# Performance work log

Hardware: AMD Instinct MI355X
Metric: run time of the kernel (lower is better)

## Reference

```python
import jax, jax.numpy as jnp
import numpy as np

B, T, F, H, FUT = 64, 512, 64, 512, 96  # batch, past len, features, hidden, future len


def setup_inputs() -> dict:
    key = jax.random.key(0)
    ks = jax.random.split(key, 19)
    s = 1.0 / np.sqrt(H)  # PyTorch LSTM/Linear init scale
    u = lambda k, shape: jax.random.uniform(k, shape, jnp.float32, -s, s)
    inp = {"input_seq": jax.random.normal(ks[0], (B, T, F), jnp.float32)}
    i = 1
    for pre in ("enc", "dec"):
        for l in range(2):
            ins = F if l == 0 else H
            inp[f"{pre}_Wih{l}"] = u(ks[i], (4 * H, ins)); i += 1
            inp[f"{pre}_Whh{l}"] = u(ks[i], (4 * H, H)); i += 1
            inp[f"{pre}_bih{l}"] = u(ks[i], (4 * H,)); i += 1
            inp[f"{pre}_bhh{l}"] = u(ks[i], (4 * H,)); i += 1
    inp["fc_W"] = u(ks[17], (F, H))
    inp["fc_b"] = u(ks[18], (F,))
    return inp


def _cell(x, h, c, Wih, Whh, bih, bhh):
    # PyTorch gate order: i, f, g, o
    g = x @ Wih.T + h @ Whh.T + bih + bhh
    i_, f_, g_, o_ = jnp.split(g, 4, axis=-1)
    c = jax.nn.sigmoid(f_) * c + jax.nn.sigmoid(i_) * jnp.tanh(g_)
    h = jax.nn.sigmoid(o_) * jnp.tanh(c)
    return h, c


def reference(input_seq, enc_Wih0, enc_Whh0, enc_bih0, enc_bhh0,
              enc_Wih1, enc_Whh1, enc_bih1, enc_bhh1,
              dec_Wih0, dec_Whh0, dec_bih0, dec_bhh0,
              dec_Wih1, dec_Whh1, dec_bih1, dec_bhh1,
              fc_W, fc_b):
    b = input_seq.shape[0]
    z = jnp.zeros((b, H), input_seq.dtype)

    def run_layer(x, Wih, Whh, bih, bhh):
        def step(carry, xt):
            h, c = _cell(xt, carry[0], carry[1], Wih, Whh, bih, bhh)
            return (h, c), h
        (h, c), ys = jax.lax.scan(step, (z, z), jnp.swapaxes(x, 0, 1))
        return jnp.swapaxes(ys, 0, 1), h, c

    # encoder (2 layers, eval mode -> no dropout)
    y0, h0, c0 = run_layer(input_seq, enc_Wih0, enc_Whh0, enc_bih0, enc_bhh0)
    _, h1, c1 = run_layer(y0, enc_Wih1, enc_Whh1, enc_bih1, enc_bhh1)

    def dec_step(carry, _):
        x, dh0, dc0, dh1, dc1 = carry
        dh0, dc0 = _cell(x, dh0, dc0, dec_Wih0, dec_Whh0, dec_bih0, dec_bhh0)
        dh1, dc1 = _cell(dh0, dh1, dc1, dec_Wih1, dec_Whh1, dec_bih1, dec_bhh1)
        out = dh1 @ fc_W.T + fc_b
        return (out, dh0, dc0, dh1, dc1), out

    dec_in = input_seq[:, -1, :]
    _, outs = jax.lax.scan(dec_step, (dec_in, h0, c0, h1, c1), None, length=FUT)
    return jnp.swapaxes(outs, 0, 1)  # [B, FUT, F]
```

## Files before the change

kernel.cpp:

```cpp
#include <hip/hip_runtime.h>
#include <stdint.h>

typedef __attribute__((ext_vector_type(8))) short short8;
typedef __attribute__((ext_vector_type(4))) float floatx4;
typedef unsigned short u16;
typedef unsigned int u32;

constexpr int BSZ = 64;
constexpr int SEQT = 512;
constexpr int FIN = 64;
constexpr int HID = 512;
constexpr int NG = 2048;
constexpr int FUTL = 96;
constexpr int K0 = FIN + HID;
constexpr int K1 = HID + HID;
constexpr int K0P = K0 + 8;
constexpr int NGRP = 256;
constexpr int NFCB = 4;
constexpr int NBLK = NGRP + NFCB;
constexpr int NTHR = 256;

constexpr int SLOT_HP = 128 * 256;
constexpr int SLOT_XP = 16 * 256;
constexpr int NSLOT_H = 65;

constexpr size_t S_W0 = (size_t)NG * K0 * 2;
constexpr size_t S_W1 = (size_t)NG * K1 * 2;
constexpr size_t S_FC = (size_t)FIN * HID * 2;

constexpr size_t OFF_WHI_E0 = 0;
constexpr size_t OFF_WLO_E0 = OFF_WHI_E0 + S_W0;
constexpr size_t OFF_WHI_E1 = OFF_WLO_E0 + S_W0;
constexpr size_t OFF_WLO_E1 = OFF_WHI_E1 + S_W1;
constexpr size_t OFF_WHI_D1 = OFF_WLO_E1 + S_W1;
constexpr size_t OFF_WLO_D1 = OFF_WHI_D1 + S_W1;
constexpr size_t OFF_WFH   = OFF_WLO_D1 + S_W1;
constexpr size_t OFF_WFL   = OFF_WFH + S_W1;
constexpr size_t OFF_FCHI  = OFF_WFL + S_W1;
constexpr size_t OFF_FCLO  = OFF_FCHI + S_FC;
constexpr size_t OFF_GX    = OFF_FCLO + S_FC;
constexpr size_t OFF_BEFF  = OFF_GX + (size_t)NG * BSZ * 4;
constexpr size_t OFF_XP    = OFF_BEFF + (size_t)NG * 4;
constexpr size_t OFF_H0P   = OFF_XP + (size_t)SEQT * SLOT_XP * 4;
constexpr size_t OFF_H1P   = OFF_H0P + (size_t)NSLOT_H * SLOT_HP * 4;
constexpr size_t OFF_CNT   = OFF_H1P + (size_t)NSLOT_H * SLOT_HP * 4;
constexpr size_t CNT_BYTES = 65536;

#define FCF(c)   ((c) + 0)
#define DONE0(c) ((c) + 256)
#define DONE1(c) ((c) + 2304)
#define GOA0(c)  ((c) + 4352)
#define GOB0(c)  ((c) + 6400)
#define GOA1(c)  ((c) + 8448)
#define GOB1(c)  ((c) + 10496)

__device__ __forceinline__ u16 f2bf(float f) {
  u32 u = __float_as_uint(f);
  u += 0x7FFFu + ((u >> 16) & 1u);
  return (u16)(u >> 16);
}
__device__ __forceinline__ float bf2f(u16 h) { return __uint_as_float(((u32)h) << 16); }
__device__ __forceinline__ u32 packsplit(float v) {
  u16 h = f2bf(v);
  u16 l = f2bf(v - bf2f(h));
  return (u32)h | ((u32)l << 16);
}

__device__ __forceinline__ float sigf(float x) { return 1.f / (1.f + __expf(-x)); }
__device__ __forceinline__ float tanh_f(float x) {
  float xx = fminf(20.f, fmaxf(-20.f, x));
  float e = __expf(-2.f * xx);
  return (1.f - e) / (1.f + e);
}

__device__ __forceinline__ floatx4 mfma3(short8 ah, short8 al, short8 bh, short8 bl, floatx4 acc) {
  acc = __builtin_amdgcn_mfma_f32_16x16x32_bf16(ah, bh, acc, 0, 0, 0);
  acc = __builtin_amdgcn_mfma_f32_16x16x32_bf16(ah, bl, acc, 0, 0, 0);
  acc = __builtin_amdgcn_mfma_f32_16x16x32_bf16(al, bh, acc, 0, 0, 0);
  return acc;
}

__device__ __forceinline__ void st_sc_u32(u32* p, u32 v) {
  asm volatile("global_store_dword %0, %1, off sc0 sc1" :: "v"(p), "v"(v) : "memory");
}
#define WAITVM0() asm volatile("s_waitcnt vmcnt(0)" ::: "memory")

#define ALD(p) __hip_atomic_load((p), __ATOMIC_RELAXED, __HIP_MEMORY_SCOPE_AGENT)
#define AST(p, v) __hip_atomic_store((p), (v), __ATOMIC_RELAXED, __HIP_MEMORY_SCOPE_AGENT)

__device__ __forceinline__ int slotof(int u) { return u < 0 ? 0 : ((u & 63) + 1); }

__device__ __forceinline__ void ld_frag(const u32* p, short8& ah, short8& al) {
  uint4 a = *(const uint4*)p;
  uint4 b = *(const uint4*)(p + 256);
  union { u32 u[4]; short8 s; } H, L;
  H.u[0] = __builtin_amdgcn_perm(a.y, a.x, 0x05040100u);
  L.u[0] = __builtin_amdgcn_perm(a.y, a.x, 0x07060302u);
  H.u[1] = __builtin_amdgcn_perm(a.w, a.z, 0x05040100u);
  L.u[1] = __builtin_amdgcn_perm(a.w, a.z, 0x07060302u);
  H.u[2] = __builtin_amdgcn_perm(b.y, b.x, 0x05040100u);
  L.u[2] = __builtin_amdgcn_perm(b.y, b.x, 0x07060302u);
  H.u[3] = __builtin_amdgcn_perm(b.w, b.z, 0x05040100u);
  L.u[3] = __builtin_amdgcn_perm(b.w, b.z, 0x07060302u);
  ah = H.s; al = L.s;
}

__global__ void k_split_pair(const float* __restrict__ Wih, const float* __restrict__ Whh,
                             int ins, int K, u16* __restrict__ hi, u16* __restrict__ lo) {
  int n = NG * K;
  for (int idx = blockIdx.x * blockDim.x + threadIdx.x; idx < n; idx += gridDim.x * blockDim.x) {
    int row = idx / K;
    int k = idx - row * K;
    float v = (k < ins) ? Wih[row * ins + k] : Whh[row * HID + (k - ins)];
    u16 h = f2bf(v);
    hi[idx] = h;
    lo[idx] = f2bf(v - bf2f(h));
  }
}

__global__ void k_split_flat(const float* __restrict__ src, u16* __restrict__ hi,
                             u16* __restrict__ lo, int n) {
  for (int idx = blockIdx.x * blockDim.x + threadIdx.x; idx < n; idx += gridDim.x * blockDim.x) {
    float v = src[idx];
    u16 h = f2bf(v);
    hi[idx] = h;
    lo[idx] = f2bf(v - bf2f(h));
  }
}

__global__ void k_fuse(const float* __restrict__ dWih0, const float* __restrict__ dWhh0,
                       const float* __restrict__ fcW,
                       u16* __restrict__ wfh, u16* __restrict__ wfl) {
  __shared__ float wr[FIN];
  const int row = blockIdx.x;
  if (threadIdx.x < FIN) wr[threadIdx.x] = dWih0[row * FIN + threadIdx.x];
  __syncthreads();
  for (int j = threadIdx.x; j < HID; j += blockDim.x) {
    float acc = 0.f;
#pragma unroll
    for (int f = 0; f < FIN; ++f) acc = fmaf(wr[f], fcW[f * HID + j], acc);
    u16 h = f2bf(acc);
    wfh[(size_t)row * K1 + j] = h;
    wfl[(size_t)row * K1 + j] = f2bf(acc - bf2f(h));
    float v2 = dWhh0[row * HID + j];
    u16 h2 = f2bf(v2);
    wfh[(size_t)row * K1 + HID + j] = h2;
    wfl[(size_t)row * K1 + HID + j] = f2bf(v2 - bf2f(h2));
  }
}

__global__ void k_gx(const float* __restrict__ dWih0, const float* __restrict__ in_seq,
                     const float* __restrict__ fcb, const float* __restrict__ bdih0,
                     const float* __restrict__ bdhh0, float* __restrict__ gx,
                     float* __restrict__ beff) {
  __shared__ float xl[BSZ * FIN];
  __shared__ float fb[FIN];
  const int row0 = blockIdx.x * 8;
  for (int i = threadIdx.x; i < BSZ * FIN; i += blockDim.x) {
    int b = i >> 6, f = i & 63;
    xl[i] = in_seq[(b * SEQT + (SEQT - 1)) * FIN + f];
  }
  if (threadIdx.x < FIN) fb[threadIdx.x] = fcb[threadIdx.x];
  __syncthreads();
  for (int i = threadIdx.x; i < 8 * BSZ; i += blockDim.x) {
    int r = row0 + (i >> 6);
    int b = i & 63;
    float acc = 0.f;
#pragma unroll 8
    for (int f = 0; f < FIN; ++f)
      acc = fmaf(dWih0[r * FIN + f], xl[(b << 6) + f] - fb[f], acc);
    gx[r * BSZ + b] = acc;
    if (b == 0) {
      float accb = 0.f;
#pragma unroll 8
      for (int f = 0; f < FIN; ++f) accb = fmaf(dWih0[r * FIN + f], fb[f], accb);
      beff[r] = bdih0[r] + bdhh0[r] + accb;
    }
  }
}

__global__ void k_pack_x(const float* __restrict__ x, u32* __restrict__ xp) {
  int n = BSZ * SEQT * FIN;
  for (int idx = blockIdx.x * blockDim.x + threadIdx.x; idx < n; idx += gridDim.x * blockDim.x) {
    int t = idx / (BSZ * FIN);
    int rem = idx - t * (BSZ * FIN);
    int b = rem >> 6;
    int f = rem & 63;
    u32 pk = packsplit(x[(b * SEQT + t) * FIN + f]);
    int off = ((f >> 2) * 64 + b) * 4 + (f & 3);
    xp[t * SLOT_XP + off] = pk;
  }
}

struct Params {
  const u16 *we0h, *we0l, *we1h, *we1l;
  const u16 *wd1h, *wd1l, *wfh, *wfl;
  const u16 *fch, *fcl;
  const u32 *xp;
  u32 *h0p, *h1p;
  const float *beih0, *behh0, *beih1, *behh1;
  const float *bdih1, *bdhh1;
  const float *gx, *beff;
  const float *fcb;
  float *out;
  u32 *cnt;
};

__device__ void master_wait(u32* own, u32 ownT) {
  if (threadIdx.x < 64) {
    int l = threadIdx.x;
    while (!__all(ALD(own + l * 16) >= ownT && ALD(own + (l + 64) * 16) >= ownT)) {}
  }
  __syncthreads();
}

__device__ void sweep128(u32* arr, u32 T) {
  if (threadIdx.x < 64) {
    int l = threadIdx.x;
    while (!__all(ALD(arr + l * 16) >= T && ALD(arr + (l + 64) * 16) >= T))
      __builtin_amdgcn_s_sleep(1);
  }
  __syncthreads();
}

__device__ __forceinline__ void worker_wait(u32* cell, u32 tok) {
  if (threadIdx.x == 0) {
    while (ALD(cell) < tok) {}
  }
  __syncthreads();
}

__device__ __forceinline__ void worker_wait_c(u32* cell, u32 tok, u32& cache) {
  if (threadIdx.x == 0 && cache < tok) {
    u32 v;
    do { v = ALD(cell); } while (v < tok);
    cache = v;
  }
  __syncthreads();
}

__device__ __forceinline__ void fcf_wait_c(u32* fcf, u32 tok, u32& cache) {
  if (threadIdx.x == 0 && cache < tok) {
    u32 m;
    do {
      u32 a = ALD(fcf), b = ALD(fcf + 16), c = ALD(fcf + 32), d = ALD(fcf + 48);
      u32 m1 = a < b ? a : b, m2 = c < d ? c : d;
      m = m1 < m2 ? m1 : m2;
    } while (m < tok);
    cache = m;
  }
  __syncthreads();
}

__device__ __forceinline__ void fence_acq() {
  __builtin_amdgcn_fence(__ATOMIC_ACQUIRE, "agent");
}

__device__ __forceinline__ void arrive(u32* cell, u32 tok) {
  WAITVM0();
  __syncthreads();
  if (threadIdx.x == 0) AST(cell, tok);
}

__device__ __forceinline__ void bcast(u32* goA, u32 tokA, u32* goBF, u32 prog) {
  const int tid = threadIdx.x;
  if (tid >= 1 && tid < 128) AST(goA + (tid << 4), tokA);
  else if (tid >= 128) AST(goBF + ((tid - 128) << 4), prog);
}

template <bool IS_L1>
__device__ void load_w_lds(const u16* __restrict__ gh, const u16* __restrict__ gl,
                           u16* wh, u16* wl, int hc) {
  constexpr int K = IS_L1 ? K1 : K0;
  for (int i = threadIdx.x; i < 16 * K; i += NTHR) {
    int rr, k;
    if (IS_L1) { rr = i >> 10; k = i & 1023; }
    else       { rr = i / K0;  k = i - rr * K0; }
    int gc = ((rr >> 2) * HID) + hc + (rr & 3);
    int dst = IS_L1 ? ((rr << 10) + ((((k >> 3) ^ rr)) << 3) + (k & 7))
                    : (rr * K0P + k);
    wh[dst] = gh[(size_t)gc * K + k];
    wl[dst] = gl[(size_t)gc * K + k];
  }
  __syncthreads();
}

template <bool IS_L1, int KBASE, int LEN>
__device__ __forceinline__ void kpart(const u32* __restrict__ sp,
                                      const u16* __restrict__ wh, const u16* __restrict__ wl,
                                      int r, int quad, int mo, floatx4& acc) {
  const int qo = quad << 3;
  constexpr int NIT = LEN / 32;
  uint4 ra[NIT], rb[NIT];
#pragma unroll
  for (int i = 0; i < NIT; ++i) {
    const u32* p = sp + (((i * 32 + qo) >> 2) << 8) + mo;
    ra[i] = *(const uint4*)p;
    rb[i] = *(const uint4*)(p + 256);
  }
#pragma unroll
  for (int i = 0; i < NIT; ++i) {
    union { u32 u[4]; short8 s; } H, L;
    H.u[0] = __builtin_amdgcn_perm(ra[i].y, ra[i].x, 0x05040100u);
    L.u[0] = __builtin_amdgcn_perm(ra[i].y, ra[i].x, 0x07060302u);
    H.u[1] = __builtin_amdgcn_perm(ra[i].w, ra[i].z, 0x05040100u);
    L.u[1] = __builtin_amdgcn_perm(ra[i].w, ra[i].z, 0x07060302u);
    H.u[2] = __builtin_amdgcn_perm(rb[i].y, rb[i].x, 0x05040100u);
    L.u[2] = __builtin_amdgcn_perm(rb[i].y, rb[i].x, 0x07060302u);
    H.u[3] = __builtin_amdgcn_perm(rb[i].w, rb[i].z, 0x05040100u);
    L.u[3] = __builtin_amdgcn_perm(rb[i].w, rb[i].z, 0x07060302u);
    const int kg = i * 32 + KBASE;
    int woff;
    if (IS_L1) { int c = (kg >> 3) + quad; woff = (r << 10) + ((c ^ r) << 3); }
    else       { woff = r * K0P + kg + qo; }
    short8 bh = *(const short8*)(wh + woff);
    short8 bl = *(const short8*)(wl + woff);
    acc = mfma3(H.s, L.s, bh, bl, acc);
  }
}

__device__ __forceinline__ void epilogue(floatx4 acc, floatx4 bs, float& creg,
                                         u32* __restrict__ oslab,
                                         const float* __restrict__ gxb) {
  const int tid = threadIdx.x, lane = tid & 63;
  const int j = lane & 3;
  const int isel = (lane >> 2) & 3;
  const int slb = lane & 48;
  float gate[4];
#pragma unroll
  for (int q = 0; q < 4; ++q) {
    const int sl = slb + (q << 2) + j;
    float t0 = __shfl(acc[0], sl, 64);
    float t1 = __shfl(acc[1], sl, 64);
    float t2 = __shfl(acc[2], sl, 64);
    float t3 = __shfl(acc[3], sl, 64);
    gate[q] = (isel == 0) ? t0 : (isel == 1) ? t1 : (isel == 2) ? t2 : t3;
  }
  if (gxb != nullptr) {
    const int bb = tid >> 2;
#pragma unroll
    for (int q = 0; q < 4; ++q) gate[q] += gxb[q * (HID * BSZ) + j * BSZ + bb];
  }
  float iv = gate[0] + bs[0];
  float fv = gate[1] + bs[1];
  float gv = gate[2] + bs[2];
  float ov = gate[3] + bs[3];
  float cn = fmaf(sigf(fv), creg, sigf(iv) * tanh_f(gv));
  float hn = sigf(ov) * tanh_f(cn);
  creg = cn;
  st_sc_u32(oslab + tid, packsplit(hn));
}

__device__ void fc_step(int t, int blkq, const u32* __restrict__ h1slot,
                        const u16* __restrict__ fh, const u16* __restrict__ fl,
                        const float* __restrict__ fcb, float* __restrict__ out) {
  const int tid = threadIdx.x, lane = tid & 63, w = tid >> 6;
  const int quad = lane >> 4, r = lane & 15;
  const int m = (w << 4) + r;
  const int qo = quad << 3;
  const int mo = m << 2;
  const int col = (blkq << 4) + r;
  floatx4 acc = {0.f, 0.f, 0.f, 0.f};
#pragma unroll
  for (int kk = 0; kk < HID; kk += 32) {
    short8 ah, al;
    ld_frag(h1slot + (((kk + qo) >> 2) << 8) + mo, ah, al);
    short8 b1 = *(const short8*)(fh + col * HID + kk + qo);
    short8 b2 = *(const short8*)(fl + col * HID + kk + qo);
    acc = mfma3(ah, al, b1, b2, acc);
  }
  float bias = fcb[col];
#pragma unroll
  for (int i = 0; i < 4; ++i) {
    int b = (w << 4) + (quad << 2) + i;
    out[(b * FUTL + t) * FIN + col] = acc[i] + bias;
  }
}

__global__ __launch_bounds__(NTHR, 1) void lstm_coop(Params p) {
  __shared__ u16 wsmem[32768];
  u16* wh = wsmem;
  u16* wl = wsmem + 16 * 1024;
  const int blk = blockIdx.x;
  const int tid = threadIdx.x;

  u32* fcf = FCF(p.cnt);
  u32* d0 = DONE0(p.cnt);
  u32* d1 = DONE1(p.cnt);

  if (blk >= NGRP) {
    const int fi = blk - NGRP;
    for (int t = 0; t < FUTL; ++t) {
      sweep128(d1, (u32)(513 + t));
      if ((t & 63) == 0) fence_acq();
      fc_step(t, fi, p.h1p + (size_t)slotof(512 + t) * SLOT_HP,
              p.fch, p.fcl, p.fcb, p.out);
      WAITVM0();
      __syncthreads();
      if (tid == 0) AST(fcf + fi * 16, (u32)(t + 1));
    }
    return;
  }

  const int grp = blk >> 7;
  const int lidx = blk & 127;
  const int hc = lidx << 2;
  const int lane = tid & 63, w = tid >> 6;
  const int quad = lane >> 4, r = lane & 15;
  const int mo = ((w << 4) + r) << 2;

  u32* goA  = grp ? GOA1(p.cnt) : GOA0(p.cnt);
  u32* goBF = grp ? GOB0(p.cnt) : GOB1(p.cnt);
  u32* myGoA = goA + lidx * 16;
  u32* myGoB = (grp ? GOB1(p.cnt) : GOB0(p.cnt)) + lidx * 16;
  u32* myDone = (grp ? d1 : d0) + lidx * 16;

  floatx4 bse, bsd;
  {
    int ch = hc + (tid & 3);
    const float* bi  = grp ? p.beih1 : p.beih0;
    const float* bh2 = grp ? p.behh1 : p.behh0;
#pragma unroll
    for (int q = 0; q < 4; ++q) {
      bse[q] = bi[q * HID + ch] + bh2[q * HID + ch];
      bsd[q] = grp ? (p.bdih1[q * HID + ch] + p.bdhh1[q * HID + ch])
                   : p.beff[q * HID + ch];
    }
  }
  float creg = 0.f;

  if (!grp) {
    u32 d1seen = 0;
    load_w_lds<false>(p.we0h, p.we0l, wh, wl, hc);
    for (int s = 0; s < SEQT; ++s) {
      u32 tok = (u32)(s + 1);
      floatx4 acc = {0.f, 0.f, 0.f, 0.f};
      if (lidx == 0) {
        master_wait(d0, (u32)s);
        if (s >= 63) worker_wait_c(myGoB, (u32)(s - 63), d1seen);
        bcast(goA, tok, goBF, (u32)s);
        if ((s & 63) == 0 && s) fence_acq();
        kpart<false, 0, FIN>(p.xp + (size_t)s * SLOT_XP, wh, wl, r, quad, mo, acc);
      } else {
        kpart<false, 0, FIN>(p.xp + (size_t)s * SLOT_XP, wh, wl, r, quad, mo, acc);
        worker_wait(myGoA, tok);
        if ((s & 63) == 0 && s) fence_acq();
      }
      kpart<false, FIN, HID>(p.h0p + (size_t)slotof(s - 1) * SLOT_HP, wh, wl, r, quad, mo, acc);
      epilogue(acc, bse, creg,
               p.h0p + (size_t)slotof(s) * SLOT_HP + (lidx << 8), nullptr);
      arrive(myDone, tok);
    }
    if (lidx == 0) {
      sweep128(d0, 512u);
      if (tid >= 128) AST(goBF + ((tid - 128) << 4), 512u);
    }
    load_w_lds<true>(p.wfh, p.wfl, wh, wl, hc);
    for (int t = 0; t < FUTL; ++t) {
      u32 tok = (u32)(513 + t);
      floatx4 acc = {0.f, 0.f, 0.f, 0.f};
      if (lidx == 0) {
        master_wait(d0, (u32)(512 + t));
        if (t == 0) worker_wait_c(myGoB, 449u, d1seen);
        bcast(goA, tok, goBF, (u32)(512 + t));
      } else {
        worker_wait(myGoA, tok);
      }
      if ((t & 63) == 0) fence_acq();
      kpart<true, 512, HID>(p.h0p + (size_t)slotof(511 + t) * SLOT_HP, wh, wl, r, quad, mo, acc);
      if (t) {
        worker_wait_c(myGoB, (u32)(512 + t), d1seen);
        kpart<true, 0, HID>(p.h1p + (size_t)slotof(511 + t) * SLOT_HP, wh, wl, r, quad, mo, acc);
      }
      epilogue(acc, bsd, creg,
               p.h0p + (size_t)slotof(512 + t) * SLOT_HP + (lidx << 8),
               (t == 0) ? (p.gx + hc * BSZ) : nullptr);
      arrive(myDone, tok);
    }
    if (lidx == 0) {
      sweep128(d0, 608u);
      if (tid >= 128) AST(goBF + ((tid - 128) << 4), 608u);
    }
  } else {
    u32 d0seen = 0;
    u32 fcseen = 0;
    load_w_lds<true>(p.we1h, p.we1l, wh, wl, hc);
    for (int t = 0; t < SEQT; ++t) {
      u32 tok = (u32)(t + 1);
      floatx4 acc = {0.f, 0.f, 0.f, 0.f};
      if (lidx == 0) {
        master_wait(d1, (u32)t);
        bcast(goA, tok, goBF, (u32)t);
        worker_wait_c(myGoB, (u32)(t + 1), d0seen);
        if ((t & 63) == 0 && t) fence_acq();
        kpart<true, 0, HID>(p.h0p + (size_t)slotof(t) * SLOT_HP, wh, wl, r, quad, mo, acc);
        kpart<true, 512, HID>(p.h1p + (size_t)slotof(t - 1) * SLOT_HP, wh, wl, r, quad, mo, acc);
      } else {
        worker_wait_c(myGoB, (u32)(t + 1), d0seen);
        if ((t & 63) == 0 && t) fence_acq();
        kpart<true, 0, HID>(p.h0p + (size_t)slotof(t) * SLOT_HP, wh, wl, r, quad, mo, acc);
        worker_wait(myGoA, tok);
        kpart<true, 512, HID>(p.h1p + (size_t)slotof(t - 1) * SLOT_HP, wh, wl, r, quad, mo, acc);
      }
      epilogue(acc, bse, creg,
               p.h1p + (size_t)slotof(t) * SLOT_HP + (lidx << 8), nullptr);
      arrive(myDone, tok);
    }
    load_w_lds<true>(p.wd1h, p.wd1l, wh, wl, hc);
    for (int t = 0; t < FUTL; ++t) {
      u32 tok = (u32)(513 + t);
      floatx4 acc = {0.f, 0.f, 0.f, 0.f};
      if (lidx == 0) {
        master_wait(d1, (u32)(512 + t));
        if (t >= 64) fcf_wait_c(fcf, (u32)(t - 63), fcseen);
        bcast(goA, tok, goBF, (u32)(512 + t));
      } else {
        worker_wait(myGoA, tok);
      }
      if ((t & 63) == 0) fence_acq();
      kpart<true, 512, HID>(p.h1p + (size_t)slotof(511 + t) * SLOT_HP, wh, wl, r, quad, mo, acc);
      worker_wait_c(myGoB, (u32)(513 + t), d0seen);
      kpart<true, 0, HID>(p.h0p + (size_t)slotof(512 + t) * SLOT_HP, wh, wl, r, quad, mo, acc);
      epilogue(acc, bsd, creg,
               p.h1p + (size_t)slotof(512 + t) * SLOT_HP + (lidx << 8), nullptr);
      arrive(myDone, tok);
    }
  }
}

extern "C" void kernel_launch(void* const* d_in, const int* in_sizes, int n_in,
                              void* d_out, int out_size, void* d_ws, size_t ws_size,
                              hipStream_t stream) {
  (void)in_sizes; (void)n_in; (void)out_size; (void)ws_size;
  const float* in_seq = (const float*)d_in[0];
  const float* eWih0 = (const float*)d_in[1];
  const float* eWhh0 = (const float*)d_in[2];
  const float* ebih0 = (const float*)d_in[3];
  const float* ebhh0 = (const float*)d_in[4];
  const float* eWih1 = (const float*)d_in[5];
  const float* eWhh1 = (const float*)d_in[6];
  const float* ebih1 = (const float*)d_in[7];
  const float* ebhh1 = (const float*)d_in[8];
  const float* dWih0 = (const float*)d_in[9];
  const float* dWhh0 = (const float*)d_in[10];
  const float* dbih0 = (const float*)d_in[11];
  const float* dbhh0 = (const float*)d_in[12];
  const float* dWih1 = (const float*)d_in[13];
  const float* dWhh1 = (const float*)d_in[14];
  const float* dbih1 = (const float*)d_in[15];
  const float* dbhh1 = (const float*)d_in[16];
  const float* fcW  = (const float*)d_in[17];
  const float* fcb  = (const float*)d_in[18];

  char* ws = (char*)d_ws;
  u16* we0h = (u16*)(ws + OFF_WHI_E0); u16* we0l = (u16*)(ws + OFF_WLO_E0);
  u16* we1h = (u16*)(ws + OFF_WHI_E1); u16* we1l = (u16*)(ws + OFF_WLO_E1);
  u16* wd1h = (u16*)(ws + OFF_WHI_D1); u16* wd1l = (u16*)(ws + OFF_WLO_D1);
  u16* wfh  = (u16*)(ws + OFF_WFH);    u16* wfl  = (u16*)(ws + OFF_WFL);
  u16* fch  = (u16*)(ws + OFF_FCHI);   u16* fcl  = (u16*)(ws + OFF_FCLO);
  float* gx   = (float*)(ws + OFF_GX);
  float* beff = (float*)(ws + OFF_BEFF);
  u32* xp   = (u32*)(ws + OFF_XP);
  u32* h0p  = (u32*)(ws + OFF_H0P);
  u32* h1p  = (u32*)(ws + OFF_H1P);
  u32* cnt  = (u32*)(ws + OFF_CNT);

  hipMemsetAsync(ws + OFF_H0P, 0, (size_t)SLOT_HP * 4, stream);
  hipMemsetAsync(ws + OFF_H1P, 0, (size_t)SLOT_HP * 4, stream);
  hipMemsetAsync(ws + OFF_CNT, 0, CNT_BYTES, stream);

  k_split_pair<<<512, 256, 0, stream>>>(eWih0, eWhh0, FIN, K0, we0h, we0l);
  k_split_pair<<<512, 256, 0, stream>>>(eWih1, eWhh1, HID, K1, we1h, we1l);
  k_split_pair<<<512, 256, 0, stream>>>(dWih1, dWhh1, HID, K1, wd1h, wd1l);
  k_split_flat<<<128, 256, 0, stream>>>(fcW, fch, fcl, FIN * HID);
  k_fuse<<<NG, 256, 0, stream>>>(dWih0, dWhh0, fcW, wfh, wfl);
  k_gx<<<256, 256, 0, stream>>>(dWih0, in_seq, fcb, dbih0, dbhh0, gx, beff);
  k_pack_x<<<1024, 256, 0, stream>>>(in_seq, xp);

  Params p;
  p.we0h = we0h; p.we0l = we0l; p.we1h = we1h; p.we1l = we1l;
  p.wd1h = wd1h; p.wd1l = wd1l; p.wfh = wfh; p.wfl = wfl;
  p.fch = fch; p.fcl = fcl;
  p.xp = xp; p.h0p = h0p; p.h1p = h1p;
  p.beih0 = ebih0; p.behh0 = ebhh0; p.beih1 = ebih1; p.behh1 = ebhh1;
  p.bdih1 = dbih1; p.bdhh1 = dbhh1;
  p.gx = gx; p.beff = beff;
  p.fcb = fcb;
  p.out = (float*)d_out;
  p.cnt = cnt;

  lstm_coop<<<dim3(NBLK), dim3(NTHR), 0, stream>>>(p);
}
```

Baseline: 3.529 ms.

## Move encoder barrier masters into dedicated idle FC blocks

The per-step barrier master role for both encoder layers moves from compute block lidx==0 to two of the FC blocks, which sit idle during the encoder. Dedicated 64-thread polling loops check completion counters and broadcast go tokens, so block 0 of each group no longer serialises waiting and broadcasting with its own compute. This adds cross-block signalling hops through the dedicated master and depends on those FC blocks being co-resident.

```diff
diff --git a/kernel.cpp b/kernel.cpp
--- a/kernel.cpp
+++ b/kernel.cpp
@@ -268,6 +268,27 @@
   else if (tid >= 128) AST(goBF + ((tid - 128) << 4), prog);
 }
 
+__device__ void enc_master(u32* own, u32* fore, bool farlag, u32* goA, u32* goBF) {
+  for (int s = 0; s < SEQT; ++s) {
+    if (threadIdx.x < 64) {
+      int l = threadIdx.x;
+      for (;;) {
+        bool ok = ALD(own + l * 16) >= (u32)s && ALD(own + (l + 64) * 16) >= (u32)s;
+        if (farlag && s >= 63) {
+          u32 ft = (u32)(s - 63);
+          ok = ok && ALD(fore + l * 16) >= ft && ALD(fore + (l + 64) * 16) >= ft;
+        }
+        if (__all(ok)) break;
+        __builtin_amdgcn_s_sleep(1);
+      }
+    }
+    __syncthreads();
+    if (threadIdx.x < 128) AST(goA + (threadIdx.x << 4), (u32)(s + 1));
+    else                   AST(goBF + ((threadIdx.x - 128) << 4), (u32)s);
+    __syncthreads();
+  }
+}
+
 template <bool IS_L1>
 __device__ void load_w_lds(const u16* __restrict__ gh, const u16* __restrict__ gl,
                            u16* wh, u16* wl, int hc) {
@@ -390,6 +411,14 @@
 
   if (blk >= NGRP) {
     const int fi = blk - NGRP;
+    if (fi == 0) {
+      enc_master(d0, d1, true, GOA0(p.cnt), GOB1(p.cnt));
+      sweep128(d0, 512u);
+      if (tid < 128) AST(GOB1(p.cnt) + (tid << 4), 512u);
+    }
+    if (fi == 1) {
+      enc_master(d1, nullptr, false, GOA1(p.cnt), GOB0(p.cnt));
+    }
     for (int t = 0; t < FUTL; ++t) {
       sweep128(d1, (u32)(513 + t));
       if ((t & 63) == 0) fence_acq();
@@ -433,27 +462,14 @@
     u32 d1seen = 0;
     load_w_lds<false>(p.we0h, p.we0l, wh, wl, hc);
     for (int s = 0; s < SEQT; ++s) {
-      u32 tok = (u32)(s + 1);
       floatx4 acc = {0.f, 0.f, 0.f, 0.f};
-      if (lidx == 0) {
-        master_wait(d0, (u32)s);
-        if (s >= 63) worker_wait_c(myGoB, (u32)(s - 63), d1seen);
-        bcast(goA, tok, goBF, (u32)s);
-        if ((s & 63) == 0 && s) fence_acq();
-        kpart<false, 0, FIN>(p.xp + (size_t)s * SLOT_XP, wh, wl, r, quad, mo, acc);
-      } else {
-        kpart<false, 0, FIN>(p.xp + (size_t)s * SLOT_XP, wh, wl, r, quad, mo, acc);
-        worker_wait(myGoA, tok);
-        if ((s & 63) == 0 && s) fence_acq();
-      }
+      kpart<false, 0, FIN>(p.xp + (size_t)s * SLOT_XP, wh, wl, r, quad, mo, acc);
+      worker_wait(myGoA, (u32)(s + 1));
+      if ((s & 63) == 0 && s) fence_acq();
       kpart<false, FIN, HID>(p.h0p + (size_t)slotof(s - 1) * SLOT_HP, wh, wl, r, quad, mo, acc);
       epilogue(acc, bse, creg,
                p.h0p + (size_t)slotof(s) * SLOT_HP + (lidx << 8), nullptr);
-      arrive(myDone, tok);
-    }
-    if (lidx == 0) {
-      sweep128(d0, 512u);
-      if (tid >= 128) AST(goBF + ((tid - 128) << 4), 512u);
+      arrive(myDone, (u32)(s + 1));
     }
     load_w_lds<true>(p.wfh, p.wfl, wh, wl, hc);
     for (int t = 0; t < FUTL; ++t) {
@@ -486,25 +502,15 @@
     u32 fcseen = 0;
     load_w_lds<true>(p.we1h, p.we1l, wh, wl, hc);
     for (int t = 0; t < SEQT; ++t) {
-      u32 tok = (u32)(t + 1);
       floatx4 acc = {0.f, 0.f, 0.f, 0.f};
-      if (lidx == 0) {
-        master_wait(d1, (u32)t);
-        bcast(goA, tok, goBF, (u32)t);
-        worker_wait_c(myGoB, (u32)(t + 1), d0seen);
-        if ((t & 63) == 0 && t) fence_acq();
-        kpart<true, 0, HID>(p.h0p + (size_t)slotof(t) * SLOT_HP, wh, wl, r, quad, mo, acc);
-        kpart<true, 512, HID>(p.h1p + (size_t)slotof(t - 1) * SLOT_HP, wh, wl, r, quad, mo, acc);
-      } else {
-        worker_wait_c(myGoB, (u32)(t + 1), d0seen);
-        if ((t & 63) == 0 && t) fence_acq();
-        kpart<true, 0, HID>(p.h0p + (size_t)slotof(t) * SLOT_HP, wh, wl, r, quad, mo, acc);
-        worker_wait(myGoA, tok);
-        kpart<true, 512, HID>(p.h1p + (size_t)slotof(t - 1) * SLOT_HP, wh, wl, r, quad, mo, acc);
-      }
+      worker_wait_c(myGoB, (u32)(t + 1), d0seen);
+      if ((t & 63) == 0 && t) fence_acq();
+      kpart<true, 0, HID>(p.h0p + (size_t)slotof(t) * SLOT_HP, wh, wl, r, quad, mo, acc);
+      worker_wait(myGoA, (u32)(t + 1));
+      kpart<true, 512, HID>(p.h1p + (size_t)slotof(t - 1) * SLOT_HP, wh, wl, r, quad, mo, acc);
       epilogue(acc, bse, creg,
                p.h1p + (size_t)slotof(t) * SLOT_HP + (lidx << 8), nullptr);
-      arrive(myDone, tok);
+      arrive(myDone, (u32)(t + 1));
     }
     load_w_lds<true>(p.wd1h, p.wd1l, wh, wl, hc);
     for (int t = 0; t < FUTL; ++t) {
```

New measurement: 3.924 ms. 11.2% more time.
